# Optimization experiments

Hardware: AMD Instinct MI355X
Metric: run time of the kernel (lower is better)

The kernel has to match this reference:

```python
import jax, jax.numpy as jnp
import numpy as np

N, TC, K, TK, D, V = 64, 256, 32, 64, 256, 32000


def setup_inputs() -> dict:
    key = jax.random.key(0)
    k1, k2, k3, k4 = jax.random.split(key, 4)
    src_tokens = jax.random.randint(k1, (N, TC), 0, V)
    know_tokens = jax.random.randint(k2, (N, K, TK), 0, V)
    ck_mask = jnp.ones((N, K), dtype=bool)
    cs_ids = jax.random.randint(k3, (N,), 0, K)
    embed = jax.random.normal(k4, (V, D), dtype=jnp.float32)
    return {
        "src_tokens": src_tokens,
        "know_tokens": know_tokens,
        "ck_mask": ck_mask,
        "cs_ids": cs_ids,
        "use_cs_ids": 0,
        "embed": embed,
    }


def reference(src_tokens, know_tokens, ck_mask, cs_ids, use_cs_ids, embed):
    d = embed.shape[1]
    # "transformer" stand-in: embedding lookup; pad token 0 defines ragged mask
    ctx_enc = embed[src_tokens]                         # [N,Tc,D]
    ctx_mask = src_tokens != 0                          # [N,Tc]
    know_enc = embed[know_tokens]                       # [N,K,Tk,D]
    know_mask = (know_tokens != 0) & ck_mask[:, :, None]  # [N,K,Tk]

    ctx_len = ctx_mask.sum(-1)                          # [N]
    know_len = know_mask.sum(-1)                        # [N,K]

    # ragged segment-sum pooling with sqrt(D * length) normalization
    ctx_use = (ctx_enc * ctx_mask[..., None]).sum(1)
    ctx_use = ctx_use / jnp.sqrt(d * jnp.maximum(ctx_len, 1).astype(ctx_use.dtype))[:, None]
    know_use = (know_enc * know_mask[..., None]).sum(2)
    know_use = know_use / jnp.sqrt(d * jnp.maximum(know_len, 1).astype(know_use.dtype))[..., None]

    # batched mv attention: score per knowledge sentence
    ck_attn = jnp.einsum('nkd,nd->nk', know_use, ctx_use)  # [N,K]

    if use_cs_ids:
        cs = cs_ids
    else:
        cs = jnp.argmax(jnp.where(ck_mask, ck_attn, -jnp.inf), axis=1)

    ck_attn = jnp.where(ck_mask, ck_attn, 0.0)          # padded like to_tensor_mask

    # gather selected knowledge span
    cs_enc = jnp.take_along_axis(know_enc, cs[:, None, None, None], axis=1)[:, 0]   # [N,Tk,D]
    cs_mask = jnp.take_along_axis(know_mask, cs[:, None, None], axis=1)[:, 0]       # [N,Tk]

    full_enc = jnp.concatenate([cs_enc, ctx_enc], axis=1)      # [N,Tk+Tc,D]
    full_mask = jnp.concatenate([cs_mask, ctx_mask], axis=1)   # [N,Tk+Tc]
    full_enc = full_enc * full_mask[..., None]                 # zero padding like to_tensor_mask
    return full_enc, full_mask, ck_attn
```

## Files before the change

kernel.cpp:

```cpp
#include <hip/hip_runtime.h>
#include <math.h>

#define N_  64
#define TC_ 256
#define K_  32
#define TK_ 64
#define D_  256
#define D4_ (D_ / 4)
#define TF_ (TK_ + TC_)

__global__ __launch_bounds__(256) void kA_ctx(
        const int* __restrict__ src, const float4* __restrict__ embed4,
        float4* __restrict__ out_enc4, float* __restrict__ out_mask,
        float4* __restrict__ ws_part4, int* __restrict__ ws_clen) {
    const int n = blockIdx.x >> 3;
    const int c = blockIdx.x & 7;
    const int tid = threadIdx.x;
    const int w = tid >> 6, l = tid & 63;

    __shared__ int toks[32];
    __shared__ float4 part[4][64];

    if (tid < 32) {
        const int tok = src[n * TC_ + c * 32 + tid];
        toks[tid] = tok;
        out_mask[n * TF_ + TK_ + c * 32 + tid] = tok ? 1.f : 0.f;
    }
    __syncthreads();

    float4 acc = {0.f, 0.f, 0.f, 0.f};
    #pragma unroll
    for (int i = 0; i < 8; ++i) {
        const int t = w * 8 + i;
        const int tok = toks[t];
        float4 v = {0.f, 0.f, 0.f, 0.f};
        if (tok) v = embed4[(size_t)tok * D4_ + l];
        out_enc4[((size_t)n * TF_ + TK_ + c * 32 + t) * D4_ + l] = v;
        acc.x += v.x; acc.y += v.y; acc.z += v.z; acc.w += v.w;
    }
    part[w][l] = acc;
    __syncthreads();

    if (w == 0) {
        float4 a = part[0][l], b = part[1][l], p2 = part[2][l], p3 = part[3][l];
        a.x += b.x + p2.x + p3.x;
        a.y += b.y + p2.y + p3.y;
        a.z += b.z + p2.z + p3.z;
        a.w += b.w + p2.w + p3.w;
        ws_part4[(size_t)(n * 8 + c) * D4_ + l] = a;
        const unsigned long long ball = __ballot(l < 32 && toks[l] != 0);
        if (l == 0) ws_clen[n * 8 + c] = __popcll(ball);
    }
}

__global__ __launch_bounds__(256) void kB_know(
        const int* __restrict__ know, const int* __restrict__ ckm,
        const float4* __restrict__ embed4,
        const float4* __restrict__ ws_part4, const int* __restrict__ ws_clen,
        float* __restrict__ out_attn, float* __restrict__ ws_score) {
    const int n = blockIdx.x >> 5;
    const int k = blockIdx.x & (K_ - 1);
    const int tid = threadIdx.x;
    const int w = tid >> 6, l = tid & 63;

    __shared__ int toks[TK_];
    __shared__ float redp[4];
    __shared__ int lk_sh;

    if (tid < TK_) toks[tid] = know[((size_t)n * K_ + k) * TK_ + tid];
    __syncthreads();

    const int ck = ckm[n * K_ + k];

    float4 ctx = {0.f, 0.f, 0.f, 0.f};
    #pragma unroll
    for (int c = 0; c < 8; ++c) {
        const float4 v = ws_part4[(size_t)(n * 8 + c) * D4_ + l];
        ctx.x += v.x; ctx.y += v.y; ctx.z += v.z; ctx.w += v.w;
    }

    float4 acc = {0.f, 0.f, 0.f, 0.f};
    if (ck) {
        #pragma unroll
        for (int i = 0; i < 16; ++i) {
            const int tok = toks[w * 16 + i];
            if (tok) {
                const float4 v = embed4[(size_t)tok * D4_ + l];
                acc.x += v.x; acc.y += v.y; acc.z += v.z; acc.w += v.w;
            }
        }
    }

    float p = acc.x * ctx.x + acc.y * ctx.y + acc.z * ctx.z + acc.w * ctx.w;
    #pragma unroll
    for (int o = 32; o > 0; o >>= 1) p += __shfl_down(p, o, 64);
    if (l == 0) redp[w] = p;
    if (w == 0) {
        const unsigned long long ball = __ballot(toks[l] != 0);
        if (l == 0) lk_sh = __popcll(ball);
    }
    __syncthreads();

    if (tid == 0) {
        const float dot = redp[0] + redp[1] + redp[2] + redp[3];
        int lc = 0;
        #pragma unroll
        for (int c = 0; c < 8; ++c) lc += ws_clen[n * 8 + c];
        if (lc < 1) lc = 1;
        int lk = ck ? lk_sh : 0;
        if (lk < 1) lk = 1;
        const float score =
            dot / (sqrtf((float)(D_ * lc)) * sqrtf((float)(D_ * lk)));
        out_attn[n * K_ + k] = ck ? score : 0.f;
        ws_score[n * K_ + k] = ck ? score : -INFINITY;
    }
}

__global__ __launch_bounds__(256) void kC_sel(
        const int* __restrict__ know, const int* __restrict__ ckm,
        const int* __restrict__ cs_ids, const int* __restrict__ use_flag,
        const float4* __restrict__ embed4, const float* __restrict__ ws_score,
        float4* __restrict__ out_enc4, float* __restrict__ out_mask) {
    const int n = blockIdx.x >> 2;
    const int c = blockIdx.x & 3;
    const int tid = threadIdx.x;
    const int w = tid >> 6, l = tid & 63;

    int cs = 0;
    if (use_flag[0]) {
        cs = cs_ids[n];
    } else {
        float best = -INFINITY;
        #pragma unroll
        for (int j = 0; j < K_; ++j) {
            const float s = ws_score[n * K_ + j];
            if (s > best) { best = s; cs = j; }
        }
    }
    const int ck = ckm[n * K_ + cs];

    __shared__ int toks[16];
    if (tid < 16) {
        const int tok = know[((size_t)n * K_ + cs) * TK_ + c * 16 + tid];
        toks[tid] = tok;
        out_mask[n * TF_ + c * 16 + tid] = (ck && tok) ? 1.f : 0.f;
    }
    __syncthreads();

    #pragma unroll
    for (int i = 0; i < 4; ++i) {
        const int t = w * 4 + i;
        const int tok = toks[t];
        float4 v = {0.f, 0.f, 0.f, 0.f};
        if (ck && tok) v = embed4[(size_t)tok * D4_ + l];
        out_enc4[((size_t)n * TF_ + c * 16 + t) * D4_ + l] = v;
    }
}

extern "C" void kernel_launch(void* const* d_in, const int* in_sizes, int n_in,
                              void* d_out, int out_size, void* d_ws, size_t ws_size,
                              hipStream_t stream) {
    const int*    src      = (const int*)d_in[0];
    const int*    know     = (const int*)d_in[1];
    const int*    ckm      = (const int*)d_in[2];
    const int*    cs_ids   = (const int*)d_in[3];
    const int*    use_flag = (const int*)d_in[4];
    const float4* embed4   = (const float4*)d_in[5];

    float*  out      = (float*)d_out;
    float4* out_enc4 = (float4*)out;
    float*  out_mask = out + (size_t)N_ * TF_ * D_;
    float*  out_attn = out_mask + (size_t)N_ * TF_;

    float4* ws_part4 = (float4*)d_ws;
    int*    ws_clen  = (int*)((float*)d_ws + (size_t)N_ * 8 * D_);
    float*  ws_score = (float*)(ws_clen + N_ * 8);

    hipLaunchKernelGGL(kA_ctx, dim3(N_ * 8), dim3(256), 0, stream,
                       src, embed4, out_enc4, out_mask, ws_part4, ws_clen);
    hipLaunchKernelGGL(kB_know, dim3(N_ * K_), dim3(256), 0, stream,
                       know, ckm, embed4, ws_part4, ws_clen, out_attn, ws_score);
    hipLaunchKernelGGL(kC_sel, dim3(N_ * 4), dim3(256), 0, stream,
                       know, ckm, cs_ids, use_flag, embed4, ws_score,
                       out_enc4, out_mask);
}
```

Baseline: 110.3 us.

## Precompute vocab-by-context scores via GEMM and gather them for knowledge attention

Reorders the dot product so each knowledge score becomes a sum of per-token entries from a precomputed P = embed · ctx table (V×N), built by a new GEMM-like kernel over the whole vocabulary. The selection kernel then gathers P entries per knowledge token instead of re-reading 256-wide embedding rows for all 2048 sentences. Context pooling now goes through atomics into a transposed buffer zeroed by a memset. This adds a 32000×256×64 FLOP pass and a large workspace, falling back to the old path if the workspace is too small.

```diff
diff --git a/kernel.cpp b/kernel.cpp
--- a/kernel.cpp
+++ b/kernel.cpp
@@ -6,19 +6,25 @@
 #define K_  32
 #define TK_ 64
 #define D_  256
-#define D4_ (D_ / 4)
-#define TF_ (TK_ + TC_)
-
-__global__ __launch_bounds__(256) void kA_ctx(
+#define D4_ 64
+#define TF_ 320
+#define V_  32000
+
+#define WS_CTXT   0
+#define WS_CLEN   (D_ * N_)
+#define WS_SCORE  (WS_CLEN + N_)
+#define WS_P      (WS_SCORE + N_ * K_)
+#define WS_FLOATS_P ((size_t)WS_P + (size_t)V_ * N_)
+
+__global__ __launch_bounds__(256) void k1_ctx(
         const int* __restrict__ src, const float4* __restrict__ embed4,
         float4* __restrict__ out_enc4, float* __restrict__ out_mask,
-        float4* __restrict__ ws_part4, int* __restrict__ ws_clen) {
+        float* __restrict__ ctxTg, int* __restrict__ clen) {
     const int n = blockIdx.x >> 3;
     const int c = blockIdx.x & 7;
-    const int tid = threadIdx.x;
-    const int w = tid >> 6, l = tid & 63;
-
-    __shared__ int toks[32];
+    const int tid = threadIdx.x, w = tid >> 6, l = tid & 63;
+
+    __shared__ int    toks[32];
     __shared__ float4 part[4][64];
 
     if (tid < 32) {
@@ -43,41 +49,134 @@
 
     if (w == 0) {
         float4 a = part[0][l], b = part[1][l], p2 = part[2][l], p3 = part[3][l];
-        a.x += b.x + p2.x + p3.x;
-        a.y += b.y + p2.y + p3.y;
-        a.z += b.z + p2.z + p3.z;
-        a.w += b.w + p2.w + p3.w;
-        ws_part4[(size_t)(n * 8 + c) * D4_ + l] = a;
+        a.x += b.x + p2.x + p3.x;  a.y += b.y + p2.y + p3.y;
+        a.z += b.z + p2.z + p3.z;  a.w += b.w + p2.w + p3.w;
+        atomicAdd(&ctxTg[(4 * l + 0) * N_ + n], a.x);
+        atomicAdd(&ctxTg[(4 * l + 1) * N_ + n], a.y);
+        atomicAdd(&ctxTg[(4 * l + 2) * N_ + n], a.z);
+        atomicAdd(&ctxTg[(4 * l + 3) * N_ + n], a.w);
         const unsigned long long ball = __ballot(l < 32 && toks[l] != 0);
-        if (l == 0) ws_clen[n * 8 + c] = __popcll(ball);
-    }
-}
-
-__global__ __launch_bounds__(256) void kB_know(
+        if (l == 0) atomicAdd(&clen[n], __popcll(ball));
+    }
+}
+
+__global__ __launch_bounds__(256) void k2_gemm(
+        const float* __restrict__ embed, const float* __restrict__ ctxTg,
+        float* __restrict__ P) {
+    const int tid = threadIdx.x, w = tid >> 6, l = tid & 63;
+    const int v0 = blockIdx.x * 32 + w * 8;
+    float acc[8] = {0.f, 0.f, 0.f, 0.f, 0.f, 0.f, 0.f, 0.f};
+    #pragma unroll
+    for (int dc = 0; dc < 4; ++dc) {
+        float ctxv[64];
+        #pragma unroll
+        for (int dd = 0; dd < 64; ++dd)
+            ctxv[dd] = ctxTg[(size_t)(dc * 64 + dd) * N_ + l];
+        #pragma unroll
+        for (int r = 0; r < 8; ++r) {
+            const int vr = __builtin_amdgcn_readfirstlane(v0 + r);
+            const float* row = embed + (size_t)vr * D_ + dc * 64;
+            #pragma unroll
+            for (int dd = 0; dd < 64; ++dd)
+                acc[r] = fmaf(row[dd], ctxv[dd], acc[r]);
+        }
+    }
+    #pragma unroll
+    for (int r = 0; r < 8; ++r)
+        P[(size_t)(v0 + r) * N_ + l] = acc[r];
+}
+
+__global__ __launch_bounds__(256) void k3_sel(
         const int* __restrict__ know, const int* __restrict__ ckm,
-        const float4* __restrict__ embed4,
-        const float4* __restrict__ ws_part4, const int* __restrict__ ws_clen,
+        const int* __restrict__ cs_ids, const int* __restrict__ use_flag,
+        const float* __restrict__ embed, const float* __restrict__ P,
+        const int* __restrict__ clen,
+        float* __restrict__ out_enc, float* __restrict__ out_mask,
+        float* __restrict__ out_attn) {
+    const int n = blockIdx.x;
+    const int tid = threadIdx.x, w = tid >> 6, l = tid & 63;
+    const float4* embed4   = (const float4*)embed;
+    float4*       out_enc4 = (float4*)out_enc;
+
+    __shared__ float sc_attn[K_], sc_arg[K_];
+    __shared__ int   toks[TK_];
+    __shared__ int   cs_sh;
+
+    const float lc_f = (float)max(clen[n], 1);
+    #pragma unroll
+    for (int j = 0; j < 8; ++j) {
+        const int k = w * 8 + j;
+        const int tok = know[((size_t)n * K_ + k) * TK_ + l];
+        float p = (tok != 0) ? P[(size_t)tok * N_ + n] : 0.f;
+        #pragma unroll
+        for (int o = 32; o > 0; o >>= 1) p += __shfl_down(p, o, 64);
+        const unsigned long long ball = __ballot(tok != 0);
+        if (l == 0) {
+            const int ck = ckm[n * K_ + k];
+            int lk = ck ? __popcll(ball) : 0;  if (lk < 1) lk = 1;
+            const float score =
+                p / (sqrtf((float)D_ * lc_f) * sqrtf((float)(D_ * lk)));
+            sc_attn[k] = ck ? score : 0.f;
+            sc_arg[k]  = ck ? score : -INFINITY;
+        }
+    }
+    __syncthreads();
+    if (tid == 0) {
+        int cs;
+        if (use_flag[0]) {
+            cs = cs_ids[n];
+        } else {
+            float best = -INFINITY; cs = 0;
+            #pragma unroll
+            for (int jj = 0; jj < K_; ++jj) {
+                const float s = sc_arg[jj];
+                if (s > best) { best = s; cs = jj; }
+            }
+        }
+        cs_sh = cs;
+    }
+    if (tid < K_) out_attn[n * K_ + tid] = sc_attn[tid];
+    __syncthreads();
+    const int cs = cs_sh;
+    const int ck = ckm[n * K_ + cs];
+    if (tid < TK_) {
+        const int tok = know[((size_t)n * K_ + cs) * TK_ + tid];
+        toks[tid] = tok;
+        out_mask[n * TF_ + tid] = (ck && tok) ? 1.f : 0.f;
+    }
+    __syncthreads();
+    #pragma unroll
+    for (int i = 0; i < 16; ++i) {
+        const int t = w * 16 + i;
+        const int tok = toks[t];
+        float4 v = {0.f, 0.f, 0.f, 0.f};
+        if (ck && tok) v = embed4[(size_t)tok * D4_ + l];
+        out_enc4[((size_t)n * TF_ + t) * D4_ + l] = v;
+    }
+}
+
+__global__ __launch_bounds__(256) void f2_kb(
+        const int* __restrict__ know, const int* __restrict__ ckm,
+        const float4* __restrict__ embed4, const float* __restrict__ ctxTg,
+        const int* __restrict__ clen,
         float* __restrict__ out_attn, float* __restrict__ ws_score) {
     const int n = blockIdx.x >> 5;
     const int k = blockIdx.x & (K_ - 1);
-    const int tid = threadIdx.x;
-    const int w = tid >> 6, l = tid & 63;
-
-    __shared__ int toks[TK_];
+    const int tid = threadIdx.x, w = tid >> 6, l = tid & 63;
+
+    __shared__ int   toks[TK_];
     __shared__ float redp[4];
-    __shared__ int lk_sh;
+    __shared__ int   lk_sh;
 
     if (tid < TK_) toks[tid] = know[((size_t)n * K_ + k) * TK_ + tid];
     __syncthreads();
-
     const int ck = ckm[n * K_ + k];
 
-    float4 ctx = {0.f, 0.f, 0.f, 0.f};
-    #pragma unroll
-    for (int c = 0; c < 8; ++c) {
-        const float4 v = ws_part4[(size_t)(n * 8 + c) * D4_ + l];
-        ctx.x += v.x; ctx.y += v.y; ctx.z += v.z; ctx.w += v.w;
-    }
+    float4 ctx;
+    ctx.x = ctxTg[(4 * l + 0) * N_ + n];
+    ctx.y = ctxTg[(4 * l + 1) * N_ + n];
+    ctx.z = ctxTg[(4 * l + 2) * N_ + n];
+    ctx.w = ctxTg[(4 * l + 3) * N_ + n];
 
     float4 acc = {0.f, 0.f, 0.f, 0.f};
     if (ck) {
@@ -90,7 +189,6 @@
             }
         }
     }
-
     float p = acc.x * ctx.x + acc.y * ctx.y + acc.z * ctx.z + acc.w * ctx.w;
     #pragma unroll
     for (int o = 32; o > 0; o >>= 1) p += __shfl_down(p, o, 64);
@@ -100,15 +198,10 @@
         if (l == 0) lk_sh = __popcll(ball);
     }
     __syncthreads();
-
     if (tid == 0) {
         const float dot = redp[0] + redp[1] + redp[2] + redp[3];
-        int lc = 0;
-        #pragma unroll
-        for (int c = 0; c < 8; ++c) lc += ws_clen[n * 8 + c];
-        if (lc < 1) lc = 1;
-        int lk = ck ? lk_sh : 0;
-        if (lk < 1) lk = 1;
+        const int lc = max(clen[n], 1);
+        int lk = ck ? lk_sh : 0;  if (lk < 1) lk = 1;
         const float score =
             dot / (sqrtf((float)(D_ * lc)) * sqrtf((float)(D_ * lk)));
         out_attn[n * K_ + k] = ck ? score : 0.f;
@@ -116,15 +209,14 @@
     }
 }
 
-__global__ __launch_bounds__(256) void kC_sel(
+__global__ __launch_bounds__(256) void f3_sel(
         const int* __restrict__ know, const int* __restrict__ ckm,
         const int* __restrict__ cs_ids, const int* __restrict__ use_flag,
         const float4* __restrict__ embed4, const float* __restrict__ ws_score,
         float4* __restrict__ out_enc4, float* __restrict__ out_mask) {
     const int n = blockIdx.x >> 2;
     const int c = blockIdx.x & 3;
-    const int tid = threadIdx.x;
-    const int w = tid >> 6, l = tid & 63;
+    const int tid = threadIdx.x, w = tid >> 6, l = tid & 63;
 
     int cs = 0;
     if (use_flag[0]) {
@@ -146,7 +238,6 @@
         out_mask[n * TF_ + c * 16 + tid] = (ck && tok) ? 1.f : 0.f;
     }
     __syncthreads();
-
     #pragma unroll
     for (int i = 0; i < 4; ++i) {
         const int t = w * 4 + i;
@@ -160,27 +251,41 @@
 extern "C" void kernel_launch(void* const* d_in, const int* in_sizes, int n_in,
                               void* d_out, int out_size, void* d_ws, size_t ws_size,
                               hipStream_t stream) {
-    const int*    src      = (const int*)d_in[0];
-    const int*    know     = (const int*)d_in[1];
-    const int*    ckm      = (const int*)d_in[2];
-    const int*    cs_ids   = (const int*)d_in[3];
-    const int*    use_flag = (const int*)d_in[4];
-    const float4* embed4   = (const float4*)d_in[5];
-
-    float*  out      = (float*)d_out;
-    float4* out_enc4 = (float4*)out;
-    float*  out_mask = out + (size_t)N_ * TF_ * D_;
-    float*  out_attn = out_mask + (size_t)N_ * TF_;
-
-    float4* ws_part4 = (float4*)d_ws;
-    int*    ws_clen  = (int*)((float*)d_ws + (size_t)N_ * 8 * D_);
-    float*  ws_score = (float*)(ws_clen + N_ * 8);
-
-    hipLaunchKernelGGL(kA_ctx, dim3(N_ * 8), dim3(256), 0, stream,
-                       src, embed4, out_enc4, out_mask, ws_part4, ws_clen);
-    hipLaunchKernelGGL(kB_know, dim3(N_ * K_), dim3(256), 0, stream,
-                       know, ckm, embed4, ws_part4, ws_clen, out_attn, ws_score);
-    hipLaunchKernelGGL(kC_sel, dim3(N_ * 4), dim3(256), 0, stream,
-                       know, ckm, cs_ids, use_flag, embed4, ws_score,
-                       out_enc4, out_mask);
-}
+    const int*   src      = (const int*)d_in[0];
+    const int*   know     = (const int*)d_in[1];
+    const int*   ckm      = (const int*)d_in[2];
+    const int*   cs_ids   = (const int*)d_in[3];
+    const int*   use_flag = (const int*)d_in[4];
+    const float* embed    = (const float*)d_in[5];
+
+    float* out      = (float*)d_out;
+    float* out_mask = out + (size_t)N_ * TF_ * D_;
+    float* out_attn = out_mask + N_ * TF_;
+
+    float* ws    = (float*)d_ws;
+    float* ctxTg = ws + WS_CTXT;
+    int*   clen  = (int*)(ws + WS_CLEN);
+    float* wsc   = ws + WS_SCORE;
+    float* P     = ws + WS_P;
+
+    hipMemsetAsync(d_ws, 0, (size_t)(WS_CLEN + N_) * sizeof(float), stream);
+
+    hipLaunchKernelGGL(k1_ctx, dim3(N_ * 8), dim3(256), 0, stream,
+                       src, (const float4*)embed, (float4*)out, out_mask,
+                       ctxTg, clen);
+
+    if (ws_size >= WS_FLOATS_P * sizeof(float)) {
+        hipLaunchKernelGGL(k2_gemm, dim3(V_ / 32), dim3(256), 0, stream,
+                           embed, ctxTg, P);
+        hipLaunchKernelGGL(k3_sel, dim3(N_), dim3(256), 0, stream,
+                           know, ckm, cs_ids, use_flag, embed, P, clen,
+                           out, out_mask, out_attn);
+    } else {
+        hipLaunchKernelGGL(f2_kb, dim3(N_ * K_), dim3(256), 0, stream,
+                           know, ckm, (const float4*)embed, ctxTg, clen,
+                           out_attn, wsc);
+        hipLaunchKernelGGL(f3_sel, dim3(N_ * 4), dim3(256), 0, stream,
+                           know, ckm, cs_ids, use_flag, (const float4*)embed,
+                           wsc, (float4*)out, out_mask);
+    }
+}
```

Result: slower. 145.4 us (+31.8%).

## Fuse context, knowledge scoring and selection into one kernel per sample

Applied to the files above, without the earlier changes.

Replaces the three kernels with one 1024-thread launch. Each of 64 blocks handles one sample end to end: it pools the context, scores all 32 knowledge sentences, takes the argmax and writes the selected span. Another 128 blocks copy the context embeddings into the output in parallel. This removes two launches and the workspace round trip, but the knowledge gather now runs on only 64 blocks, so parallelism and latency hiding drop sharply. Each wave loops serially over 128 token rows.

```diff
diff --git a/kernel.cpp b/kernel.cpp
--- a/kernel.cpp
+++ b/kernel.cpp
@@ -6,181 +6,165 @@
 #define K_  32
 #define TK_ 64
 #define D_  256
-#define D4_ (D_ / 4)
-#define TF_ (TK_ + TC_)
+#define D4_ 64
+#define TF_ 320
+#define V_  32000
 
-__global__ __launch_bounds__(256) void kA_ctx(
-        const int* __restrict__ src, const float4* __restrict__ embed4,
-        float4* __restrict__ out_enc4, float* __restrict__ out_mask,
-        float4* __restrict__ ws_part4, int* __restrict__ ws_clen) {
-    const int n = blockIdx.x >> 3;
-    const int c = blockIdx.x & 7;
-    const int tid = threadIdx.x;
-    const int w = tid >> 6, l = tid & 63;
+__global__ __launch_bounds__(1024) void cke_all(
+        const int* __restrict__ src, const int* __restrict__ know,
+        const int* __restrict__ ckm, const int* __restrict__ cs_ids,
+        const int* __restrict__ use_flag, const float* __restrict__ embed,
+        float* __restrict__ out) {
+    const int tid = threadIdx.x, w = tid >> 6, l = tid & 63;
 
-    __shared__ int toks[32];
-    __shared__ float4 part[4][64];
+    float* out_mask = out + (size_t)N_ * TF_ * D_;
+    float* out_attn = out_mask + N_ * TF_;
+    const float4* embed4   = (const float4*)embed;
+    float4*       out_enc4 = (float4*)out;
 
-    if (tid < 32) {
-        const int tok = src[n * TC_ + c * 32 + tid];
-        toks[tid] = tok;
-        out_mask[n * TF_ + TK_ + c * 32 + tid] = tok ? 1.f : 0.f;
+    if (blockIdx.x >= N_) {
+        const int b = blockIdx.x - N_;
+        const int n = b >> 1, c = b & 1;
+        __shared__ int toks[128];
+        if (tid < 128) {
+            const int tok = src[n * TC_ + c * 128 + tid];
+            toks[tid] = tok;
+            out_mask[n * TF_ + TK_ + c * 128 + tid] = tok ? 1.f : 0.f;
+        }
+        __syncthreads();
+        #pragma unroll
+        for (int i = 0; i < 8; ++i) {
+            const int t = w * 8 + i;
+            const int tok = toks[t];
+            float4 v = {0.f, 0.f, 0.f, 0.f};
+            if (tok) v = embed4[(size_t)tok * D4_ + l];
+            out_enc4[((size_t)n * TF_ + TK_ + c * 128 + t) * D4_ + l] = v;
+        }
+        return;
     }
+
+    const int n = blockIdx.x;
+
+    __shared__ int    ctoks[TC_];
+    __shared__ int    ktoks[K_ * TK_];
+    __shared__ float4 part[16][64];
+    __shared__ float4 ctx4[64];
+    __shared__ int    wcnt[16];
+    __shared__ float  sc_attn[K_], sc_arg[K_];
+    __shared__ int    cs_sh, clen_sh;
+
+    if (tid < TC_) ctoks[tid] = src[n * TC_ + tid];
+    #pragma unroll
+    for (int i = tid; i < K_ * TK_; i += 1024)
+        ktoks[i] = know[(size_t)n * K_ * TK_ + i];
     __syncthreads();
 
-    float4 acc = {0.f, 0.f, 0.f, 0.f};
-    #pragma unroll
-    for (int i = 0; i < 8; ++i) {
-        const int t = w * 8 + i;
-        const int tok = toks[t];
-        float4 v = {0.f, 0.f, 0.f, 0.f};
-        if (tok) v = embed4[(size_t)tok * D4_ + l];
-        out_enc4[((size_t)n * TF_ + TK_ + c * 32 + t) * D4_ + l] = v;
-        acc.x += v.x; acc.y += v.y; acc.z += v.z; acc.w += v.w;
-    }
-    part[w][l] = acc;
-    __syncthreads();
-
-    if (w == 0) {
-        float4 a = part[0][l], b = part[1][l], p2 = part[2][l], p3 = part[3][l];
-        a.x += b.x + p2.x + p3.x;
-        a.y += b.y + p2.y + p3.y;
-        a.z += b.z + p2.z + p3.z;
-        a.w += b.w + p2.w + p3.w;
-        ws_part4[(size_t)(n * 8 + c) * D4_ + l] = a;
-        const unsigned long long ball = __ballot(l < 32 && toks[l] != 0);
-        if (l == 0) ws_clen[n * 8 + c] = __popcll(ball);
-    }
-}
-
-__global__ __launch_bounds__(256) void kB_know(
-        const int* __restrict__ know, const int* __restrict__ ckm,
-        const float4* __restrict__ embed4,
-        const float4* __restrict__ ws_part4, const int* __restrict__ ws_clen,
-        float* __restrict__ out_attn, float* __restrict__ ws_score) {
-    const int n = blockIdx.x >> 5;
-    const int k = blockIdx.x & (K_ - 1);
-    const int tid = threadIdx.x;
-    const int w = tid >> 6, l = tid & 63;
-
-    __shared__ int toks[TK_];
-    __shared__ float redp[4];
-    __shared__ int lk_sh;
-
-    if (tid < TK_) toks[tid] = know[((size_t)n * K_ + k) * TK_ + tid];
-    __syncthreads();
-
-    const int ck = ckm[n * K_ + k];
-
-    float4 ctx = {0.f, 0.f, 0.f, 0.f};
-    #pragma unroll
-    for (int c = 0; c < 8; ++c) {
-        const float4 v = ws_part4[(size_t)(n * 8 + c) * D4_ + l];
-        ctx.x += v.x; ctx.y += v.y; ctx.z += v.z; ctx.w += v.w;
-    }
-
-    float4 acc = {0.f, 0.f, 0.f, 0.f};
-    if (ck) {
+    {
+        float4 acc = {0.f, 0.f, 0.f, 0.f};
         #pragma unroll
         for (int i = 0; i < 16; ++i) {
-            const int tok = toks[w * 16 + i];
+            const int tok = ctoks[w * 16 + i];
             if (tok) {
                 const float4 v = embed4[(size_t)tok * D4_ + l];
                 acc.x += v.x; acc.y += v.y; acc.z += v.z; acc.w += v.w;
             }
         }
+        part[w][l] = acc;
+        const unsigned long long ball = __ballot(l < 16 && ctoks[w * 16 + l] != 0);
+        if (l == 0) wcnt[w] = __popcll(ball);
     }
+    __syncthreads();
+    if (tid < 64) {
+        float4 s = {0.f, 0.f, 0.f, 0.f};
+        #pragma unroll
+        for (int wv = 0; wv < 16; ++wv) {
+            const float4 v = part[wv][tid];
+            s.x += v.x; s.y += v.y; s.z += v.z; s.w += v.w;
+        }
+        ctx4[tid] = s;
+    }
+    if (tid == 0) {
+        int c = 0;
+        #pragma unroll
+        for (int i = 0; i < 16; ++i) c += wcnt[i];
+        clen_sh = c;
+    }
+    __syncthreads();
 
-    float p = acc.x * ctx.x + acc.y * ctx.y + acc.z * ctx.z + acc.w * ctx.w;
-    #pragma unroll
-    for (int o = 32; o > 0; o >>= 1) p += __shfl_down(p, o, 64);
-    if (l == 0) redp[w] = p;
-    if (w == 0) {
-        const unsigned long long ball = __ballot(toks[l] != 0);
-        if (l == 0) lk_sh = __popcll(ball);
+    {
+        const float4 cx = ctx4[l];
+        #pragma unroll
+        for (int j = 0; j < 2; ++j) {
+            const int kk = w * 2 + j;
+            float4 acc = {0.f, 0.f, 0.f, 0.f};
+            #pragma unroll 8
+            for (int t = 0; t < TK_; ++t) {
+                const int tok = ktoks[kk * TK_ + t];
+                if (tok) {
+                    const float4 v = embed4[(size_t)tok * D4_ + l];
+                    acc.x += v.x; acc.y += v.y; acc.z += v.z; acc.w += v.w;
+                }
+            }
+            float p = acc.x * cx.x + acc.y * cx.y + acc.z * cx.z + acc.w * cx.w;
+            #pragma unroll
+            for (int o = 32; o > 0; o >>= 1) p += __shfl_down(p, o, 64);
+            const unsigned long long ball = __ballot(ktoks[kk * TK_ + l] != 0);
+            if (l == 0) {
+                const int ck = ckm[n * K_ + kk];
+                int lk = ck ? __popcll(ball) : 0;  if (lk < 1) lk = 1;
+                const int lc = max(clen_sh, 1);
+                const float score =
+                    p / (sqrtf((float)(D_ * lc)) * sqrtf((float)(D_ * lk)));
+                sc_attn[kk] = ck ? score : 0.f;
+                sc_arg[kk]  = ck ? score : -INFINITY;
+            }
+        }
     }
     __syncthreads();
 
     if (tid == 0) {
-        const float dot = redp[0] + redp[1] + redp[2] + redp[3];
-        int lc = 0;
-        #pragma unroll
-        for (int c = 0; c < 8; ++c) lc += ws_clen[n * 8 + c];
-        if (lc < 1) lc = 1;
-        int lk = ck ? lk_sh : 0;
-        if (lk < 1) lk = 1;
-        const float score =
-            dot / (sqrtf((float)(D_ * lc)) * sqrtf((float)(D_ * lk)));
-        out_attn[n * K_ + k] = ck ? score : 0.f;
-        ws_score[n * K_ + k] = ck ? score : -INFINITY;
+        int cs;
+        if (use_flag[0]) {
+            cs = cs_ids[n];
+        } else {
+            float best = -INFINITY; cs = 0;
+            #pragma unroll
+            for (int jj = 0; jj < K_; ++jj) {
+                const float s = sc_arg[jj];
+                if (s > best) { best = s; cs = jj; }
+            }
+        }
+        cs_sh = cs;
     }
-}
-
-__global__ __launch_bounds__(256) void kC_sel(
-        const int* __restrict__ know, const int* __restrict__ ckm,
-        const int* __restrict__ cs_ids, const int* __restrict__ use_flag,
-        const float4* __restrict__ embed4, const float* __restrict__ ws_score,
-        float4* __restrict__ out_enc4, float* __restrict__ out_mask) {
-    const int n = blockIdx.x >> 2;
-    const int c = blockIdx.x & 3;
-    const int tid = threadIdx.x;
-    const int w = tid >> 6, l = tid & 63;
-
-    int cs = 0;
-    if (use_flag[0]) {
-        cs = cs_ids[n];
-    } else {
-        float best = -INFINITY;
-        #pragma unroll
-        for (int j = 0; j < K_; ++j) {
-            const float s = ws_score[n * K_ + j];
-            if (s > best) { best = s; cs = j; }
-        }
-    }
-    const int ck = ckm[n * K_ + cs];
-
-    __shared__ int toks[16];
-    if (tid < 16) {
-        const int tok = know[((size_t)n * K_ + cs) * TK_ + c * 16 + tid];
-        toks[tid] = tok;
-        out_mask[n * TF_ + c * 16 + tid] = (ck && tok) ? 1.f : 0.f;
-    }
+    if (tid < K_) out_attn[n * K_ + tid] = sc_attn[tid];
     __syncthreads();
 
+    const int cs = cs_sh;
+    const int ck = ckm[n * K_ + cs];
+    if (tid < TK_) {
+        const int tok = ktoks[cs * TK_ + tid];
+        out_mask[n * TF_ + tid] = (ck && tok) ? 1.f : 0.f;
+    }
     #pragma unroll
     for (int i = 0; i < 4; ++i) {
         const int t = w * 4 + i;
-        const int tok = toks[t];
+        const int tok = ktoks[cs * TK_ + t];
         float4 v = {0.f, 0.f, 0.f, 0.f};
         if (ck && tok) v = embed4[(size_t)tok * D4_ + l];
-        out_enc4[((size_t)n * TF_ + c * 16 + t) * D4_ + l] = v;
+        out_enc4[((size_t)n * TF_ + t) * D4_ + l] = v;
     }
 }
 
 extern "C" void kernel_launch(void* const* d_in, const int* in_sizes, int n_in,
                               void* d_out, int out_size, void* d_ws, size_t ws_size,
                               hipStream_t stream) {
-    const int*    src      = (const int*)d_in[0];
-    const int*    know     = (const int*)d_in[1];
-    const int*    ckm      = (const int*)d_in[2];
-    const int*    cs_ids   = (const int*)d_in[3];
-    const int*    use_flag = (const int*)d_in[4];
-    const float4* embed4   = (const float4*)d_in[5];
+    const int*   src      = (const int*)d_in[0];
+    const int*   know     = (const int*)d_in[1];
+    const int*   ckm      = (const int*)d_in[2];
+    const int*   cs_ids   = (const int*)d_in[3];
+    const int*   use_flag = (const int*)d_in[4];
+    const float* embed    = (const float*)d_in[5];
 
-    float*  out      = (float*)d_out;
-    float4* out_enc4 = (float4*)out;
-    float*  out_mask = out + (size_t)N_ * TF_ * D_;
-    float*  out_attn = out_mask + (size_t)N_ * TF_;
-
-    float4* ws_part4 = (float4*)d_ws;
-    int*    ws_clen  = (int*)((float*)d_ws + (size_t)N_ * 8 * D_);
-    float*  ws_score = (float*)(ws_clen + N_ * 8);
-
-    hipLaunchKernelGGL(kA_ctx, dim3(N_ * 8), dim3(256), 0, stream,
-                       src, embed4, out_enc4, out_mask, ws_part4, ws_clen);
-    hipLaunchKernelGGL(kB_know, dim3(N_ * K_), dim3(256), 0, stream,
-                       know, ckm, embed4, ws_part4, ws_clen, out_attn, ws_score);
-    hipLaunchKernelGGL(kC_sel, dim3(N_ * 4), dim3(256), 0, stream,
-                       know, ckm, cs_ids, use_flag, embed4, ws_score,
-                       out_enc4, out_mask);
+    hipLaunchKernelGGL(cke_all, dim3(N_ * 3), dim3(1024), 0, stream,
+                       src, know, ckm, cs_ids, use_flag, embed, (float*)d_out);
 }
```

Result: slower. 139.2 us (+26.2%).
